# Optimization experiments

Hardware: AMD Instinct MI355X
Metric: run time of the kernel (lower is better)

The kernel has to match this reference:

```python
import jax, jax.numpy as jnp
import numpy as np

N = 50000
E = 800000
IN_CH = 128
OUT_CH = 32
HEADS = 10
NEG_SLOPE = 0.2
NUM_GRAPHS = 512


def gat_layer(x, W, a_src, a_dst, b, src, dst, heads, out_ch):
    n = x.shape[0]
    h = (x @ W).reshape(n, heads, out_ch)            # [N,H,C]
    e_src = jnp.einsum('nhc,hc->nh', h, a_src)       # [N,H]
    e_dst = jnp.einsum('nhc,hc->nh', h, a_dst)       # [N,H]
    alpha = jax.nn.leaky_relu(e_src[src] + e_dst[dst], negative_slope=NEG_SLOPE)  # [E,H]
    amax = jax.ops.segment_max(alpha, dst, num_segments=n)
    amax = jnp.where(jnp.isneginf(amax), 0.0, amax)
    ex = jnp.exp(alpha - amax[dst])                   # [E,H]
    denom = jax.ops.segment_sum(ex, dst, num_segments=n)
    coef = ex / (denom[dst] + 1e-16)                  # segment softmax over incoming edges
    msg = h[src] * coef[:, :, None]                   # [E,H,C]
    out = jax.ops.segment_sum(msg, dst, num_segments=n)
    return out.reshape(n, heads * out_ch) + b


def setup_inputs() -> dict:
    key = jax.random.key(0)
    ks = jax.random.split(key, 12)
    x = jax.random.normal(ks[0], (N, IN_CH), dtype=jnp.float32)
    edge_index = jax.random.randint(ks[1], (2, E), 0, N, dtype=jnp.int32)
    batch = jnp.sort(jax.random.randint(ks[2], (N,), 0, NUM_GRAPHS, dtype=jnp.int32))
    s1 = 1.0 / np.sqrt(IN_CH)
    s2 = 1.0 / np.sqrt(HEADS * OUT_CH)
    s3 = 1.0 / np.sqrt(OUT_CH)
    W1 = jax.random.uniform(ks[3], (IN_CH, HEADS * OUT_CH), minval=-s1, maxval=s1, dtype=jnp.float32)
    a_src1 = jax.random.uniform(ks[4], (HEADS, OUT_CH), minval=-s3, maxval=s3, dtype=jnp.float32)
    a_dst1 = jax.random.uniform(ks[5], (HEADS, OUT_CH), minval=-s3, maxval=s3, dtype=jnp.float32)
    b1 = jnp.zeros((HEADS * OUT_CH,), dtype=jnp.float32)
    W2 = jax.random.uniform(ks[6], (HEADS * OUT_CH, OUT_CH), minval=-s2, maxval=s2, dtype=jnp.float32)
    a_src2 = jax.random.uniform(ks[7], (1, OUT_CH), minval=-s3, maxval=s3, dtype=jnp.float32)
    a_dst2 = jax.random.uniform(ks[8], (1, OUT_CH), minval=-s3, maxval=s3, dtype=jnp.float32)
    b2 = jnp.zeros((OUT_CH,), dtype=jnp.float32)
    fc_w = jax.random.uniform(ks[9], (OUT_CH, OUT_CH), minval=-s3, maxval=s3, dtype=jnp.float32)
    fc_b = jax.random.uniform(ks[10], (OUT_CH,), minval=-s3, maxval=s3, dtype=jnp.float32)
    return {
        'x': x, 'edge_index': edge_index, 'batch': batch, 'num_graphs': NUM_GRAPHS,
        'W1': W1, 'a_src1': a_src1, 'a_dst1': a_dst1, 'b1': b1,
        'W2': W2, 'a_src2': a_src2, 'a_dst2': a_dst2, 'b2': b2,
        'fc_w': fc_w, 'fc_b': fc_b,
    }


def reference(x, edge_index, batch, num_graphs, W1, a_src1, a_dst1, b1, W2, a_src2, a_dst2, b2, fc_w, fc_b):
    src, dst = edge_index[0], edge_index[1]
    h = gat_layer(x, W1, a_src1, a_dst1, b1, src, dst, HEADS, OUT_CH)
    h = jax.nn.elu(h)                                  # dropout = identity (eval)
    h = gat_layer(h, W2, a_src2, a_dst2, b2, src, dst, 1, OUT_CH)
    h = jax.nn.elu(h)
    pooled = jax.ops.segment_max(h, batch, num_segments=num_graphs)  # global max pool
    pooled = jnp.where(jnp.isneginf(pooled), 0.0, pooled)
    out = jax.nn.relu(pooled @ fc_w + fc_b)
    return out
```

## Files before the change

### kernel.cpp

```cpp
#include <hip/hip_runtime.h>

#define N_NODES 50000
#define N_EDGES 800000
#define IN_CH   128
#define OUT_CH  32
#define HEADS   10
#define HC      320
#define N_GRAPHS 512
#define NEG_SLOPE 0.2f
#define NBLK_SCAN 196

typedef __attribute__((ext_vector_type(8))) short bf16x8;
typedef __attribute__((ext_vector_type(4))) float f32x4;
typedef __attribute__((ext_vector_type(4))) unsigned short usx4;

__device__ __forceinline__ unsigned fmap(float f) {
  unsigned u = __float_as_uint(f);
  return (u & 0x80000000u) ? ~u : (u | 0x80000000u);
}
__device__ __forceinline__ float funmap(unsigned u) {
  u = (u & 0x80000000u) ? (u ^ 0x80000000u) : ~u;
  return __uint_as_float(u);
}
__device__ __forceinline__ float leaky(float a) {
  return a > 0.f ? a : NEG_SLOPE * a;
}
__device__ __forceinline__ unsigned short f2bf(float f) {
  unsigned u = __float_as_uint(f);
  return (unsigned short)((u + 0x7FFFu + ((u >> 16) & 1u)) >> 16);
}
__device__ __forceinline__ float bf2f(unsigned short b) {
  return __uint_as_float(((unsigned)b) << 16);
}
__device__ __forceinline__ float bflo(unsigned u) { return __uint_as_float(u << 16); }
__device__ __forceinline__ float bfhi(unsigned u) { return __uint_as_float(u & 0xFFFF0000u); }
__device__ __forceinline__ void store_split_nt(unsigned short* __restrict__ ph,
                                               unsigned short* __restrict__ pl,
                                               size_t idx, float v) {
  unsigned short h = f2bf(v);
  unsigned short l = f2bf(v - bf2f(h));
  __builtin_nontemporal_store(h, ph + idx);
  __builtin_nontemporal_store(l, pl + idx);
}
__device__ __forceinline__ float elu(float v) {
  return v > 0.f ? v : expm1f(v);
}

__global__ __launch_bounds__(256) void hist_k(const int* __restrict__ ei,
                                              int* __restrict__ deg) {
  int e = blockIdx.x * 256 + threadIdx.x;
  if (e < N_EDGES) atomicAdd(&deg[ei[N_EDGES + e]], 1);
}

__global__ __launch_bounds__(256) void scan_blk(const int* __restrict__ deg,
                                                int* __restrict__ roff,
                                                int* __restrict__ bsum) {
  __shared__ int s[256];
  int i = blockIdx.x * 256 + threadIdx.x;
  int v = (i < N_NODES) ? deg[i] : 0;
  s[threadIdx.x] = v;
  __syncthreads();
  #pragma unroll
  for (int o = 1; o < 256; o <<= 1) {
    int t = (threadIdx.x >= o) ? s[threadIdx.x - o] : 0;
    __syncthreads();
    s[threadIdx.x] += t;
    __syncthreads();
  }
  if (i < N_NODES) roff[i] = s[threadIdx.x] - v;
  if (threadIdx.x == 255) bsum[blockIdx.x] = s[255];
}

__global__ __launch_bounds__(256) void scan_top(int* __restrict__ bsum) {
  __shared__ int s[256];
  int i = threadIdx.x;
  int v = (i < NBLK_SCAN) ? bsum[i] : 0;
  s[i] = v;
  __syncthreads();
  #pragma unroll
  for (int o = 1; o < 256; o <<= 1) {
    int t = (i >= o) ? s[i - o] : 0;
    __syncthreads();
    s[i] += t;
    __syncthreads();
  }
  if (i < NBLK_SCAN) bsum[i] = s[i] - v;
}

__global__ __launch_bounds__(256) void scan_add(int* __restrict__ roff,
                                                const int* __restrict__ bsum) {
  int i = blockIdx.x * 256 + threadIdx.x;
  if (i < N_NODES) roff[i] += bsum[blockIdx.x];
  if (i == 0) roff[N_NODES] = N_EDGES;
}

__global__ __launch_bounds__(256) void scatter_k(const int* __restrict__ ei,
                                                 const int* __restrict__ roff,
                                                 int* __restrict__ cursor,
                                                 int* __restrict__ ssrc) {
  int e = blockIdx.x * 256 + threadIdx.x;
  if (e >= N_EDGES) return;
  int dst = ei[N_EDGES + e];
  int pos = roff[dst] + atomicAdd(&cursor[dst], 1);
  ssrc[pos] = ei[e];
}

__global__ __launch_bounds__(256) void conv_w(const float* __restrict__ W1,
                                              const float* __restrict__ W2,
                                              unsigned short* __restrict__ W1hT,
                                              unsigned short* __restrict__ W1lT,
                                              unsigned short* __restrict__ W2hT,
                                              unsigned short* __restrict__ W2lT) {
  int i = blockIdx.x * 256 + threadIdx.x;
  if (i < IN_CH * HC) {
    int n = i >> 7, k = i & 127;
    float v = W1[(size_t)k * HC + n];
    unsigned short h = f2bf(v);
    W1hT[i] = h; W1lT[i] = f2bf(v - bf2f(h));
  } else {
    int j = i - IN_CH * HC;
    if (j < OUT_CH * HC) {
      int c = j / HC, k = j - c * HC;
      float v = W2[(size_t)k * OUT_CH + c];
      unsigned short h = f2bf(v);
      W2hT[j] = h; W2lT[j] = f2bf(v - bf2f(h));
    }
  }
}

__global__ __launch_bounds__(256) void gemm1_mfma(const float* __restrict__ X,
                                                  const unsigned short* __restrict__ WhT,
                                                  const unsigned short* __restrict__ WlT,
                                                  unsigned short* __restrict__ Hb) {
  const int wave = threadIdx.x >> 6;
  const int lane = threadIdx.x & 63;
  const int row0 = blockIdx.x * 64 + wave * 16;
  const int r = lane & 15;
  const int kg = lane >> 4;
  int arow = row0 + r; if (arow >= N_NODES) arow = N_NODES - 1;
  const float* xrow = X + (size_t)arow * IN_CH + kg * 8;
  const unsigned short* wb = WhT + (size_t)r * IN_CH + kg * 8;
  const unsigned short* lb = WlT + (size_t)r * IN_CH + kg * 8;
  f32x4 acc[20];
  #pragma unroll
  for (int c = 0; c < 20; c++) acc[c] = f32x4{0.f, 0.f, 0.f, 0.f};
  #pragma unroll
  for (int k0 = 0; k0 < IN_CH; k0 += 32) {
    float4 u = *reinterpret_cast<const float4*>(xrow + k0);
    float4 w = *reinterpret_cast<const float4*>(xrow + k0 + 4);
    float uv0 = u.x, uv1 = u.y, uv2 = u.z, uv3 = u.w;
    float uv4 = w.x, uv5 = w.y, uv6 = w.z, uv7 = w.w;
    bf16x8 ah, al;
    unsigned short hh;
    hh = f2bf(uv0); ah[0] = (short)hh; al[0] = (short)f2bf(uv0 - bf2f(hh));
    hh = f2bf(uv1); ah[1] = (short)hh; al[1] = (short)f2bf(uv1 - bf2f(hh));
    hh = f2bf(uv2); ah[2] = (short)hh; al[2] = (short)f2bf(uv2 - bf2f(hh));
    hh = f2bf(uv3); ah[3] = (short)hh; al[3] = (short)f2bf(uv3 - bf2f(hh));
    hh = f2bf(uv4); ah[4] = (short)hh; al[4] = (short)f2bf(uv4 - bf2f(hh));
    hh = f2bf(uv5); ah[5] = (short)hh; al[5] = (short)f2bf(uv5 - bf2f(hh));
    hh = f2bf(uv6); ah[6] = (short)hh; al[6] = (short)f2bf(uv6 - bf2f(hh));
    hh = f2bf(uv7); ah[7] = (short)hh; al[7] = (short)f2bf(uv7 - bf2f(hh));
    #pragma unroll
    for (int c = 0; c < 20; c++) {
      bf16x8 bh = *reinterpret_cast<const bf16x8*>(wb + (size_t)c * 16 * IN_CH + k0);
      bf16x8 bl = *reinterpret_cast<const bf16x8*>(lb + (size_t)c * 16 * IN_CH + k0);
      acc[c] = __builtin_amdgcn_mfma_f32_16x16x32_bf16(ah, bh, acc[c], 0, 0, 0);
      acc[c] = __builtin_amdgcn_mfma_f32_16x16x32_bf16(ah, bl, acc[c], 0, 0, 0);
      acc[c] = __builtin_amdgcn_mfma_f32_16x16x32_bf16(al, bh, acc[c], 0, 0, 0);
    }
  }
  const int crow0 = row0 + kg * 4;
  #pragma unroll
  for (int c = 0; c < 20; c++) {
    const int ccol = c * 16 + r;
    #pragma unroll
    for (int t = 0; t < 4; t++) {
      int rr = crow0 + t;
      if (rr < N_NODES) Hb[(size_t)rr * HC + ccol] = f2bf(acc[c][t]);
    }
  }
}

__global__ __launch_bounds__(256) void gemm2_mfma(const unsigned short* __restrict__ Ah,
                                                  const unsigned short* __restrict__ Al,
                                                  const unsigned short* __restrict__ WhT,
                                                  const unsigned short* __restrict__ WlT,
                                                  const float* __restrict__ a_src2,
                                                  const float* __restrict__ a_dst2,
                                                  float* __restrict__ H,
                                                  float* __restrict__ es,
                                                  float* __restrict__ ed) {
  const int wave = threadIdx.x >> 6;
  const int lane = threadIdx.x & 63;
  const int row0 = blockIdx.x * 64 + wave * 16;
  const int r = lane & 15;
  const int kg = lane >> 4;
  int arow = row0 + r; if (arow >= N_NODES) arow = N_NODES - 1;
  const unsigned short* ah_p = Ah + (size_t)arow * HC + kg * 8;
  const unsigned short* al_p = Al + (size_t)arow * HC + kg * 8;
  const unsigned short* wb = WhT + (size_t)r * HC + kg * 8;
  const unsigned short* lb = WlT + (size_t)r * HC + kg * 8;
  f32x4 acc[2];
  acc[0] = f32x4{0.f, 0.f, 0.f, 0.f};
  acc[1] = f32x4{0.f, 0.f, 0.f, 0.f};
  #pragma unroll
  for (int k0 = 0; k0 < HC; k0 += 32) {
    bf16x8 ah = *reinterpret_cast<const bf16x8*>(ah_p + k0);
    bf16x8 al = *reinterpret_cast<const bf16x8*>(al_p + k0);
    #pragma unroll
    for (int c = 0; c < 2; c++) {
      bf16x8 bh = *reinterpret_cast<const bf16x8*>(wb + (size_t)c * 16 * HC + k0);
      bf16x8 bl = *reinterpret_cast<const bf16x8*>(lb + (size_t)c * 16 * HC + k0);
      acc[c] = __builtin_amdgcn_mfma_f32_16x16x32_bf16(ah, bh, acc[c], 0, 0, 0);
      acc[c] = __builtin_amdgcn_mfma_f32_16x16x32_bf16(ah, bl, acc[c], 0, 0, 0);
      acc[c] = __builtin_amdgcn_mfma_f32_16x16x32_bf16(al, bh, acc[c], 0, 0, 0);
    }
  }
  const int crow0 = row0 + kg * 4;
  #pragma unroll
  for (int c = 0; c < 2; c++) {
    const int ccol = c * 16 + r;
    #pragma unroll
    for (int t = 0; t < 4; t++) {
      int rr = crow0 + t;
      if (rr < N_NODES) H[(size_t)rr * OUT_CH + ccol] = acc[c][t];
    }
  }
  const float as0 = a_src2[r], as1 = a_src2[16 + r];
  const float ad0 = a_dst2[r], ad1 = a_dst2[16 + r];
  float pe[4], pd[4];
  #pragma unroll
  for (int t = 0; t < 4; t++) {
    pe[t] = acc[0][t] * as0 + acc[1][t] * as1;
    pd[t] = acc[0][t] * ad0 + acc[1][t] * ad1;
  }
  #pragma unroll
  for (int o = 1; o < 16; o <<= 1) {
    #pragma unroll
    for (int t = 0; t < 4; t++) {
      pe[t] += __shfl_xor(pe[t], o);
      pd[t] += __shfl_xor(pd[t], o);
    }
  }
  if (r == 0) {
    #pragma unroll
    for (int t = 0; t < 4; t++) {
      int rr = crow0 + t;
      if (rr < N_NODES) { es[rr] = pe[t]; ed[rr] = pd[t]; }
    }
  }
}

__global__ __launch_bounds__(256) void edot1(const unsigned short* __restrict__ h1b,
                                             const float* __restrict__ a_src,
                                             const float* __restrict__ a_dst,
                                             float* __restrict__ es,
                                             float* __restrict__ ed) {
  int idx = blockIdx.x * 256 + threadIdx.x;
  if (idx >= N_NODES * HEADS) return;
  int n = idx / HEADS, h = idx - n * HEADS;
  const uint4* hp = reinterpret_cast<const uint4*>(h1b + (size_t)n * HC + h * OUT_CH);
  const float2* ap = reinterpret_cast<const float2*>(a_src + h * OUT_CH);
  const float2* bp = reinterpret_cast<const float2*>(a_dst + h * OUT_CH);
  float s = 0.f, d = 0.f;
  #pragma unroll
  for (int q = 0; q < 4; q++) {
    uint4 u = hp[q];
    unsigned w[4] = {u.x, u.y, u.z, u.w};
    #pragma unroll
    for (int k = 0; k < 4; k++) {
      float lo = bflo(w[k]), hi = bfhi(w[k]);
      float2 av = ap[q * 4 + k], bv = bp[q * 4 + k];
      s += lo * av.x + hi * av.y;
      d += lo * bv.x + hi * bv.y;
    }
  }
  es[idx] = s; ed[idx] = d;
}

__global__ __launch_bounds__(256) void agg1(const int* __restrict__ roff,
                                            const int* __restrict__ ssrc,
                                            const float* __restrict__ es,
                                            const float* __restrict__ ed,
                                            const unsigned short* __restrict__ h1b,
                                            const float* __restrict__ b1,
                                            unsigned short* __restrict__ acth,
                                            unsigned short* __restrict__ actl) {
  __shared__ float lds[4][64][11];
  const int n = (blockIdx.x * 256 + threadIdx.x) >> 6;
  if (n >= N_NODES) return;
  const int wslot = threadIdx.x >> 6;
  const int lane = threadIdx.x & 63;
  const int beg = roff[n];
  const int deg = roff[n + 1] - beg;

  if (deg == 0) {
    #pragma unroll
    for (int q = 0; q < 5; q++) {
      float v = elu(b1[lane + 64 * q]);
      store_split_nt(acth, actl, (size_t)n * HC + lane + 64 * q, v);
    }
    return;
  }

  if (deg <= 64) {
    const int active = (lane < deg);
    const int src = ssrc[beg + (active ? lane : 0)];
    #pragma unroll
    for (int p = 0; p < 5; p++) {
      float2 edp = *reinterpret_cast<const float2*>(ed + n * 10 + 2 * p);
      float2 esp = *reinterpret_cast<const float2*>(es + src * 10 + 2 * p);
      lds[wslot][lane][2 * p]     = active ? expf(leaky(esp.x + edp.x)) : 0.f;
      lds[wslot][lane][2 * p + 1] = active ? expf(leaky(esp.y + edp.y)) : 0.f;
    }
    lds[wslot][lane][10] = __int_as_float(src * (HC * 2));

    const int half = lane >> 5;
    const int lc = lane & 31;
    const int hm = lc >> 2;
    const int ht = 8 + (lc >> 4);
    float accm[8] = {};
    float acct0 = 0.f, acct1 = 0.f, dm = 0.f, dt = 0.f;
    const int dege = (deg + 1) & ~1;
    const char* basem = reinterpret_cast<const char*>(h1b + 8 * lc);
    const char* baset = reinterpret_cast<const char*>(h1b + 256 + 2 * lc);
    for (int j = 0; j < dege; j += 2) {
      const int e = j + half;
      int off = __float_as_int(lds[wslot][e][10]);
      float cm = lds[wslot][e][hm];
      float ct = lds[wslot][e][ht];
      uint4 v = *reinterpret_cast<const uint4*>(basem + off);
      unsigned t = *reinterpret_cast<const unsigned*>(baset + off);
      unsigned w0 = v.x, w1 = v.y, w2 = v.z, w3 = v.w;
      accm[0] = fmaf(bflo(w0), cm, accm[0]);
      accm[1] = fmaf(bfhi(w0), cm, accm[1]);
      accm[2] = fmaf(bflo(w1), cm, accm[2]);
      accm[3] = fmaf(bfhi(w1), cm, accm[3]);
      accm[4] = fmaf(bflo(w2), cm, accm[4]);
      accm[5] = fmaf(bfhi(w2), cm, accm[5]);
      accm[6] = fmaf(bflo(w3), cm, accm[6]);
      accm[7] = fmaf(bfhi(w3), cm, accm[7]);
      acct0 = fmaf(bflo(t), ct, acct0);
      acct1 = fmaf(bfhi(t), ct, acct1);
      dm += cm;
      dt += ct;
    }
    #pragma unroll
    for (int k = 0; k < 8; k++) accm[k] += __shfl_xor(accm[k], 32);
    acct0 += __shfl_xor(acct0, 32);
    acct1 += __shfl_xor(acct1, 32);
    dm += __shfl_xor(dm, 32);
    dt += __shfl_xor(dt, 32);

    if (lane < 32) {
      const float invm = 1.f / (dm + 1e-16f);
      const size_t base = (size_t)n * HC;
      usx4 sh0, sl0, sh1, sl1;
      float vv;
      unsigned short hh;
      vv = elu(accm[0] * invm + b1[8 * lc + 0]); hh = f2bf(vv); sh0[0] = hh; sl0[0] = f2bf(vv - bf2f(hh));
      vv = elu(accm[1] * invm + b1[8 * lc + 1]); hh = f2bf(vv); sh0[1] = hh; sl0[1] = f2bf(vv - bf2f(hh));
      vv = elu(accm[2] * invm + b1[8 * lc + 2]); hh = f2bf(vv); sh0[2] = hh; sl0[2] = f2bf(vv - bf2f(hh));
      vv = elu(accm[3] * invm + b1[8 * lc + 3]); hh = f2bf(vv); sh0[3] = hh; sl0[3] = f2bf(vv - bf2f(hh));
      vv = elu(accm[4] * invm + b1[8 * lc + 4]); hh = f2bf(vv); sh1[0] = hh; sl1[0] = f2bf(vv - bf2f(hh));
      vv = elu(accm[5] * invm + b1[8 * lc + 5]); hh = f2bf(vv); sh1[1] = hh; sl1[1] = f2bf(vv - bf2f(hh));
      vv = elu(accm[6] * invm + b1[8 * lc + 6]); hh = f2bf(vv); sh1[2] = hh; sl1[2] = f2bf(vv - bf2f(hh));
      vv = elu(accm[7] * invm + b1[8 * lc + 7]); hh = f2bf(vv); sh1[3] = hh; sl1[3] = f2bf(vv - bf2f(hh));
      __builtin_nontemporal_store(sh0, reinterpret_cast<usx4*>(acth + base + 8 * lc));
      __builtin_nontemporal_store(sh1, reinterpret_cast<usx4*>(acth + base + 8 * lc + 4));
      __builtin_nontemporal_store(sl0, reinterpret_cast<usx4*>(actl + base + 8 * lc));
      __builtin_nontemporal_store(sl1, reinterpret_cast<usx4*>(actl + base + 8 * lc + 4));
      const float invt = 1.f / (dt + 1e-16f);
      unsigned tph, tpl;
      unsigned short h0, h1v, l0, l1v;
      vv = elu(acct0 * invt + b1[256 + 2 * lc + 0]); h0 = f2bf(vv); l0 = f2bf(vv - bf2f(h0));
      vv = elu(acct1 * invt + b1[256 + 2 * lc + 1]); h1v = f2bf(vv); l1v = f2bf(vv - bf2f(h1v));
      tph = (unsigned)h0 | ((unsigned)h1v << 16);
      tpl = (unsigned)l0 | ((unsigned)l1v << 16);
      __builtin_nontemporal_store(tph, reinterpret_cast<unsigned*>(acth + base + 256 + 2 * lc));
      __builtin_nontemporal_store(tpl, reinterpret_cast<unsigned*>(actl + base + 256 + 2 * lc));
    }
  } else {
    const int hb = lane >> 5;
    float acc[5] = {};
    float edv[5], m2[5];
    #pragma unroll
    for (int q = 0; q < 5; q++) { edv[q] = ed[n * 10 + 2 * q + hb]; m2[q] = -1e30f; }
    for (int j = beg; j < beg + deg; j++) {
      int src = ssrc[j];
      #pragma unroll
      for (int q = 0; q < 5; q++)
        m2[q] = fmaxf(m2[q], leaky(es[src * 10 + 2 * q + hb] + edv[q]));
    }
    float d2[5] = {};
    for (int j = beg; j < beg + deg; j++) {
      int src = ssrc[j];
      const unsigned short* hrow = h1b + (size_t)src * HC + lane;
      #pragma unroll
      for (int q = 0; q < 5; q++) {
        float ex = expf(leaky(es[src * 10 + 2 * q + hb] + edv[q]) - m2[q]);
        acc[q] = fmaf(bf2f(hrow[64 * q]), ex, acc[q]);
        d2[q] += ex;
      }
    }
    #pragma unroll
    for (int q = 0; q < 5; q++) {
      float v = elu(acc[q] / (d2[q] + 1e-16f) + b1[lane + 64 * q]);
      store_split_nt(acth, actl, (size_t)n * HC + lane + 64 * q, v);
    }
  }
}

__global__ __launch_bounds__(256) void agg2(const int* __restrict__ roff,
                                            const int* __restrict__ ssrc,
                                            const float* __restrict__ es,
                                            const float* __restrict__ ed,
                                            const float* __restrict__ h2,
                                            const float* __restrict__ b2,
                                            const int* __restrict__ batch,
                                            unsigned* __restrict__ pooled) {
  __shared__ float lds[4][64][2];
  const int n = (blockIdx.x * 256 + threadIdx.x) >> 6;
  if (n >= N_NODES) return;
  const int wslot = threadIdx.x >> 6;
  const int lane = threadIdx.x & 63;
  const int c = lane & 31;
  const int hb = lane >> 5;
  const int beg = roff[n];
  const int deg = roff[n + 1] - beg;
  const int g = batch[n];

  if (deg == 0) {
    if (lane < 32) {
      float v = elu(b2[c]);
      atomicMax(&pooled[g * OUT_CH + c], fmap(v));
    }
    return;
  }

  float acc = 0.f, dacc = 0.f, dtot;

  if (deg <= 64) {
    const int active = (lane < deg);
    const int src = ssrc[beg + (active ? lane : 0)];
    const float edv = ed[n];
    float ex = active ? expf(leaky(es[src] + edv)) : 0.f;
    lds[wslot][lane][0] = ex;
    lds[wslot][lane][1] = __int_as_float(src * (OUT_CH * 4));
    const char* baseh = reinterpret_cast<const char*>(h2 + c);
    int j = hb;
    for (; j + 6 < deg; j += 8) {
      int o0 = __float_as_int(lds[wslot][j + 0][1]);
      int o1 = __float_as_int(lds[wslot][j + 2][1]);
      int o2 = __float_as_int(lds[wslot][j + 4][1]);
      int o3 = __float_as_int(lds[wslot][j + 6][1]);
      float c0 = lds[wslot][j + 0][0];
      float c1 = lds[wslot][j + 2][0];
      float c2 = lds[wslot][j + 4][0];
      float c3 = lds[wslot][j + 6][0];
      float v0 = *reinterpret_cast<const float*>(baseh + o0);
      float v1 = *reinterpret_cast<const float*>(baseh + o1);
      float v2 = *reinterpret_cast<const float*>(baseh + o2);
      float v3 = *reinterpret_cast<const float*>(baseh + o3);
      acc = fmaf(v0, c0, acc);
      acc = fmaf(v1, c1, acc);
      acc = fmaf(v2, c2, acc);
      acc = fmaf(v3, c3, acc);
      dacc += c0 + c1 + c2 + c3;
    }
    for (; j < deg; j += 2) {
      int oj = __float_as_int(lds[wslot][j][1]);
      float cj = lds[wslot][j][0];
      acc = fmaf(*reinterpret_cast<const float*>(baseh + oj), cj, acc);
      dacc += cj;
    }
    acc += __shfl_xor(acc, 32);
    dacc += __shfl_xor(dacc, 32);
    dtot = dacc;
  } else {
    const float edv = ed[n];
    float m = -1e30f;
    for (int j = beg; j < beg + deg; j++)
      m = fmaxf(m, leaky(es[ssrc[j]] + edv));
    float d = 0.f;
    for (int j = beg + hb; j < beg + deg; j += 2) {
      int src = ssrc[j];
      float ex = expf(leaky(es[src] + edv) - m);
      acc = fmaf(h2[(size_t)src * OUT_CH + c], ex, acc);
      d += ex;
    }
    acc += __shfl_xor(acc, 32);
    d += __shfl_xor(d, 32);
    dtot = d;
  }

  if (lane < 32) {
    float v = elu(acc / (dtot + 1e-16f) + b2[c]);
    atomicMax(&pooled[g * OUT_CH + c], fmap(v));
  }
}

__global__ __launch_bounds__(256) void final_k(const unsigned* __restrict__ pooled,
                                               const float* __restrict__ fc_w,
                                               const float* __restrict__ fc_b,
                                               float* __restrict__ out) {
  int idx = blockIdx.x * 256 + threadIdx.x;
  if (idx >= N_GRAPHS * OUT_CH) return;
  int g = idx >> 5, c = idx & 31;
  float s = fc_b[c];
  #pragma unroll
  for (int k = 0; k < OUT_CH; k++) {
    unsigned u = pooled[g * OUT_CH + k];
    float p = (u == 0u) ? 0.f : funmap(u);
    s += p * fc_w[k * OUT_CH + c];
  }
  out[idx] = s > 0.f ? s : 0.f;
}

extern "C" void kernel_launch(void* const* d_in, const int* in_sizes, int n_in,
                              void* d_out, int out_size, void* d_ws, size_t ws_size,
                              hipStream_t stream) {
  const float* x      = (const float*)d_in[0];
  const int*   ei     = (const int*)d_in[1];
  const int*   batch  = (const int*)d_in[2];
  const float* W1     = (const float*)d_in[4];
  const float* a_src1 = (const float*)d_in[5];
  const float* a_dst1 = (const float*)d_in[6];
  const float* b1     = (const float*)d_in[7];
  const float* W2     = (const float*)d_in[8];
  const float* a_src2 = (const float*)d_in[9];
  const float* a_dst2 = (const float*)d_in[10];
  const float* b2     = (const float*)d_in[11];
  const float* fc_w   = (const float*)d_in[12];
  const float* fc_b   = (const float*)d_in[13];
  float* out = (float*)d_out;

  char* ws = (char*)d_ws;
  unsigned short* h1b = (unsigned short*)(ws);
  float* h2   = (float*)(ws);
  unsigned short* acth = (unsigned short*)(ws + 64000000);
  unsigned short* actl = (unsigned short*)(ws + 96000000);
  char*  S    = ws + 128000000;
  int*   ssrc   = (int*)(S);
  int*   roff   = (int*)(S + 3200000);
  int*   deg    = (int*)(S + 3400064);
  int*   cursor = (int*)(S + 3600064);
  unsigned short* W1hT = (unsigned short*)(S + 3400064);
  unsigned short* W1lT = (unsigned short*)(S + 3400064 + 81920);
  unsigned short* W2hT = (unsigned short*)(S + 3400064 + 163840);
  unsigned short* W2lT = (unsigned short*)(S + 3400064 + 184320);
  float* es1    = (float*)(S + 3800064);
  float* ed1    = (float*)(S + 5800064);
  int*   bsum   = (int*)(S + 7800064);
  unsigned* pooled = (unsigned*)(S + 7801600);
  float* es2 = es1; float* ed2 = ed1;

  hipMemsetAsync(deg, 0, (size_t)N_NODES * 4, stream);
  hipMemsetAsync(cursor, 0, (size_t)N_NODES * 4, stream);
  hist_k   <<<(N_EDGES + 255) / 256, 256, 0, stream>>>(ei, deg);
  scan_blk <<<NBLK_SCAN, 256, 0, stream>>>(deg, roff, bsum);
  scan_top <<<1, 256, 0, stream>>>(bsum);
  scan_add <<<NBLK_SCAN, 256, 0, stream>>>(roff, bsum);
  scatter_k<<<(N_EDGES + 255) / 256, 256, 0, stream>>>(ei, roff, cursor, ssrc);

  conv_w<<<(IN_CH * HC + OUT_CH * HC + 255) / 256, 256, 0, stream>>>(
      W1, W2, W1hT, W1lT, W2hT, W2lT);

  gemm1_mfma<<<(N_NODES + 63) / 64, 256, 0, stream>>>(x, W1hT, W1lT, h1b);
  edot1<<<(N_NODES * HEADS + 255) / 256, 256, 0, stream>>>(h1b, a_src1, a_dst1, es1, ed1);
  agg1 <<<(N_NODES * 64 + 255) / 256, 256, 0, stream>>>(roff, ssrc, es1, ed1, h1b, b1,
                                                        acth, actl);

  hipMemsetAsync(pooled, 0, (size_t)N_GRAPHS * OUT_CH * 4, stream);
  gemm2_mfma<<<(N_NODES + 63) / 64, 256, 0, stream>>>(acth, actl, W2hT, W2lT,
                                                      a_src2, a_dst2, h2, es2, ed2);
  agg2 <<<(N_NODES * 64 + 255) / 256, 256, 0, stream>>>(roff, ssrc, es2, ed2, h2, b2,
                                                        batch, pooled);
  final_k<<<(N_GRAPHS * OUT_CH + 255) / 256, 256, 0, stream>>>(pooled, fc_w, fc_b, out);
}
```

Baseline: 366.3 us.

## Fold attention projections into GEMM1 and drop nontemporal stores

Precomputes W1·a_src and W1·a_dst as 20 extra weight columns so gemm1 produces the per-head attention logits directly, removing the separate edot1 kernel that re-read the whole bf16 h1 tensor. The GEMM gains two extra 16-column tiles of MFMA work and more accumulator registers. Separately, agg1's activation stores switch from nontemporal to normal stores so gemm2 may hit in cache. Logits now come from a split-bf16 product rather than a dot over rounded h, slightly changing numerics.

```diff
diff --git a/kernel.cpp b/kernel.cpp
--- a/kernel.cpp
+++ b/kernel.cpp
@@ -34,13 +34,12 @@
 }
 __device__ __forceinline__ float bflo(unsigned u) { return __uint_as_float(u << 16); }
 __device__ __forceinline__ float bfhi(unsigned u) { return __uint_as_float(u & 0xFFFF0000u); }
-__device__ __forceinline__ void store_split_nt(unsigned short* __restrict__ ph,
-                                               unsigned short* __restrict__ pl,
-                                               size_t idx, float v) {
+__device__ __forceinline__ void store_split(unsigned short* __restrict__ ph,
+                                            unsigned short* __restrict__ pl,
+                                            size_t idx, float v) {
   unsigned short h = f2bf(v);
-  unsigned short l = f2bf(v - bf2f(h));
-  __builtin_nontemporal_store(h, ph + idx);
-  __builtin_nontemporal_store(l, pl + idx);
+  ph[idx] = h;
+  pl[idx] = f2bf(v - bf2f(h));
 }
 __device__ __forceinline__ float elu(float v) {
   return v > 0.f ? v : expm1f(v);
@@ -128,10 +127,33 @@
   }
 }
 
+__global__ __launch_bounds__(256) void conv_wa(const float* __restrict__ W1,
+                                               const float* __restrict__ a_src1,
+                                               const float* __restrict__ a_dst1,
+                                               unsigned short* __restrict__ W1hT,
+                                               unsigned short* __restrict__ W1lT) {
+  int i = blockIdx.x * 256 + threadIdx.x;
+  if (i >= 32 * IN_CH) return;
+  int j = i >> 7, k = i & 127;
+  float v = 0.f;
+  if (j < 20) {
+    int head = (j < 10) ? j : (j - 10);
+    const float* a = (j < 10) ? (a_src1 + head * OUT_CH) : (a_dst1 + head * OUT_CH);
+    const float* wrow = W1 + (size_t)k * HC + head * OUT_CH;
+    #pragma unroll
+    for (int c = 0; c < OUT_CH; c++) v += wrow[c] * a[c];
+  }
+  unsigned short h = f2bf(v);
+  W1hT[(size_t)(HC + j) * IN_CH + k] = h;
+  W1lT[(size_t)(HC + j) * IN_CH + k] = f2bf(v - bf2f(h));
+}
+
 __global__ __launch_bounds__(256) void gemm1_mfma(const float* __restrict__ X,
                                                   const unsigned short* __restrict__ WhT,
                                                   const unsigned short* __restrict__ WlT,
-                                                  unsigned short* __restrict__ Hb) {
+                                                  unsigned short* __restrict__ Hb,
+                                                  float* __restrict__ es,
+                                                  float* __restrict__ ed) {
   const int wave = threadIdx.x >> 6;
   const int lane = threadIdx.x & 63;
   const int row0 = blockIdx.x * 64 + wave * 16;
@@ -141,9 +163,9 @@
   const float* xrow = X + (size_t)arow * IN_CH + kg * 8;
   const unsigned short* wb = WhT + (size_t)r * IN_CH + kg * 8;
   const unsigned short* lb = WlT + (size_t)r * IN_CH + kg * 8;
-  f32x4 acc[20];
-  #pragma unroll
-  for (int c = 0; c < 20; c++) acc[c] = f32x4{0.f, 0.f, 0.f, 0.f};
+  f32x4 acc[22];
+  #pragma unroll
+  for (int c = 0; c < 22; c++) acc[c] = f32x4{0.f, 0.f, 0.f, 0.f};
   #pragma unroll
   for (int k0 = 0; k0 < IN_CH; k0 += 32) {
     float4 u = *reinterpret_cast<const float4*>(xrow + k0);
@@ -161,7 +183,7 @@
     hh = f2bf(uv6); ah[6] = (short)hh; al[6] = (short)f2bf(uv6 - bf2f(hh));
     hh = f2bf(uv7); ah[7] = (short)hh; al[7] = (short)f2bf(uv7 - bf2f(hh));
     #pragma unroll
-    for (int c = 0; c < 20; c++) {
+    for (int c = 0; c < 22; c++) {
       bf16x8 bh = *reinterpret_cast<const bf16x8*>(wb + (size_t)c * 16 * IN_CH + k0);
       bf16x8 bl = *reinterpret_cast<const bf16x8*>(lb + (size_t)c * 16 * IN_CH + k0);
       acc[c] = __builtin_amdgcn_mfma_f32_16x16x32_bf16(ah, bh, acc[c], 0, 0, 0);
@@ -177,6 +199,16 @@
     for (int t = 0; t < 4; t++) {
       int rr = crow0 + t;
       if (rr < N_NODES) Hb[(size_t)rr * HC + ccol] = f2bf(acc[c][t]);
+    }
+  }
+  #pragma unroll
+  for (int t = 0; t < 4; t++) {
+    int rr = crow0 + t;
+    if (rr < N_NODES) {
+      float v20 = acc[20][t];
+      if (r < 10) es[rr * 10 + r] = v20;
+      else        ed[rr * 10 + (r - 10)] = v20;
+      if (r < 4)  ed[rr * 10 + 6 + r] = acc[21][t];
     }
   }
 }
@@ -251,33 +283,6 @@
   }
 }
 
-__global__ __launch_bounds__(256) void edot1(const unsigned short* __restrict__ h1b,
-                                             const float* __restrict__ a_src,
-                                             const float* __restrict__ a_dst,
-                                             float* __restrict__ es,
-                                             float* __restrict__ ed) {
-  int idx = blockIdx.x * 256 + threadIdx.x;
-  if (idx >= N_NODES * HEADS) return;
-  int n = idx / HEADS, h = idx - n * HEADS;
-  const uint4* hp = reinterpret_cast<const uint4*>(h1b + (size_t)n * HC + h * OUT_CH);
-  const float2* ap = reinterpret_cast<const float2*>(a_src + h * OUT_CH);
-  const float2* bp = reinterpret_cast<const float2*>(a_dst + h * OUT_CH);
-  float s = 0.f, d = 0.f;
-  #pragma unroll
-  for (int q = 0; q < 4; q++) {
-    uint4 u = hp[q];
-    unsigned w[4] = {u.x, u.y, u.z, u.w};
-    #pragma unroll
-    for (int k = 0; k < 4; k++) {
-      float lo = bflo(w[k]), hi = bfhi(w[k]);
-      float2 av = ap[q * 4 + k], bv = bp[q * 4 + k];
-      s += lo * av.x + hi * av.y;
-      d += lo * bv.x + hi * bv.y;
-    }
-  }
-  es[idx] = s; ed[idx] = d;
-}
-
 __global__ __launch_bounds__(256) void agg1(const int* __restrict__ roff,
                                             const int* __restrict__ ssrc,
                                             const float* __restrict__ es,
@@ -298,7 +303,7 @@
     #pragma unroll
     for (int q = 0; q < 5; q++) {
       float v = elu(b1[lane + 64 * q]);
-      store_split_nt(acth, actl, (size_t)n * HC + lane + 64 * q, v);
+      store_split(acth, actl, (size_t)n * HC + lane + 64 * q, v);
     }
     return;
   }
@@ -366,10 +371,10 @@
       vv = elu(accm[5] * invm + b1[8 * lc + 5]); hh = f2bf(vv); sh1[1] = hh; sl1[1] = f2bf(vv - bf2f(hh));
       vv = elu(accm[6] * invm + b1[8 * lc + 6]); hh = f2bf(vv); sh1[2] = hh; sl1[2] = f2bf(vv - bf2f(hh));
       vv = elu(accm[7] * invm + b1[8 * lc + 7]); hh = f2bf(vv); sh1[3] = hh; sl1[3] = f2bf(vv - bf2f(hh));
-      __builtin_nontemporal_store(sh0, reinterpret_cast<usx4*>(acth + base + 8 * lc));
-      __builtin_nontemporal_store(sh1, reinterpret_cast<usx4*>(acth + base + 8 * lc + 4));
-      __builtin_nontemporal_store(sl0, reinterpret_cast<usx4*>(actl + base + 8 * lc));
-      __builtin_nontemporal_store(sl1, reinterpret_cast<usx4*>(actl + base + 8 * lc + 4));
+      *reinterpret_cast<usx4*>(acth + base + 8 * lc) = sh0;
+      *reinterpret_cast<usx4*>(acth + base + 8 * lc + 4) = sh1;
+      *reinterpret_cast<usx4*>(actl + base + 8 * lc) = sl0;
+      *reinterpret_cast<usx4*>(actl + base + 8 * lc + 4) = sl1;
       const float invt = 1.f / (dt + 1e-16f);
       unsigned tph, tpl;
       unsigned short h0, h1v, l0, l1v;
@@ -377,8 +382,8 @@
       vv = elu(acct1 * invt + b1[256 + 2 * lc + 1]); h1v = f2bf(vv); l1v = f2bf(vv - bf2f(h1v));
       tph = (unsigned)h0 | ((unsigned)h1v << 16);
       tpl = (unsigned)l0 | ((unsigned)l1v << 16);
-      __builtin_nontemporal_store(tph, reinterpret_cast<unsigned*>(acth + base + 256 + 2 * lc));
-      __builtin_nontemporal_store(tpl, reinterpret_cast<unsigned*>(actl + base + 256 + 2 * lc));
+      *reinterpret_cast<unsigned*>(acth + base + 256 + 2 * lc) = tph;
+      *reinterpret_cast<unsigned*>(actl + base + 256 + 2 * lc) = tpl;
     }
   } else {
     const int hb = lane >> 5;
@@ -406,7 +411,7 @@
     #pragma unroll
     for (int q = 0; q < 5; q++) {
       float v = elu(acc[q] / (d2[q] + 1e-16f) + b1[lane + 64 * q]);
-      store_split_nt(acth, actl, (size_t)n * HC + lane + 64 * q, v);
+      store_split(acth, actl, (size_t)n * HC + lane + 64 * q, v);
     }
   }
 }
@@ -546,9 +551,9 @@
   int*   deg    = (int*)(S + 3400064);
   int*   cursor = (int*)(S + 3600064);
   unsigned short* W1hT = (unsigned short*)(S + 3400064);
-  unsigned short* W1lT = (unsigned short*)(S + 3400064 + 81920);
-  unsigned short* W2hT = (unsigned short*)(S + 3400064 + 163840);
-  unsigned short* W2lT = (unsigned short*)(S + 3400064 + 184320);
+  unsigned short* W1lT = (unsigned short*)(S + 3400064 + 90112);
+  unsigned short* W2hT = (unsigned short*)(S + 3400064 + 180224);
+  unsigned short* W2lT = (unsigned short*)(S + 3400064 + 200704);
   float* es1    = (float*)(S + 3800064);
   float* ed1    = (float*)(S + 5800064);
   int*   bsum   = (int*)(S + 7800064);
@@ -565,9 +570,10 @@
 
   conv_w<<<(IN_CH * HC + OUT_CH * HC + 255) / 256, 256, 0, stream>>>(
       W1, W2, W1hT, W1lT, W2hT, W2lT);
-
-  gemm1_mfma<<<(N_NODES + 63) / 64, 256, 0, stream>>>(x, W1hT, W1lT, h1b);
-  edot1<<<(N_NODES * HEADS + 255) / 256, 256, 0, stream>>>(h1b, a_src1, a_dst1, es1, ed1);
+  conv_wa<<<(32 * IN_CH + 255) / 256, 256, 0, stream>>>(
+      W1, a_src1, a_dst1, W1hT, W1lT);
+
+  gemm1_mfma<<<(N_NODES + 63) / 64, 256, 0, stream>>>(x, W1hT, W1lT, h1b, es1, ed1);
   agg1 <<<(N_NODES * 64 + 255) / 256, 256, 0, stream>>>(roff, ssrc, es1, ed1, h1b, b1,
                                                         acth, actl);
 
```

Measured after the change: 350.6 us (median of 2 runs). 1.05x faster.
